# Optimization experiments

Measured on AMD Instinct MI355X. Metric: run time of the kernel, lower is better.

## Reference

```python
import jax, jax.numpy as jnp
import numpy as np

GZ = 15          # grid size (gz)
C_IN = 4         # grid channels == R output dim
N_DEEP = 16      # number of stride-1 conv blocks after conv1
BN_EPS = 1e-5


def _bn_eval(x, g, b):
    # eval-mode BatchNorm2d with running_mean=0, running_var=1
    s = g / jnp.sqrt(1.0 + BN_EPS)
    return x * s[None, :, None, None] + b[None, :, None, None]


def _conv(x, w, b, stride):
    y = jax.lax.conv_general_dilated(
        x, w, window_strides=(stride, stride), padding=[(2, 2), (2, 2)],
        dimension_numbers=('NCHW', 'OIHW', 'NCHW'))
    return y + b[None, :, None, None]


def _cnn(x, conv1_w, conv1_b, bn1_g, bn1_b, convs_w, convs_b, bns_g, bns_b):
    x = jax.nn.elu(_bn_eval(_conv(x, conv1_w, conv1_b, 2), bn1_g, bn1_b))
    for i in range(N_DEEP):  # fixed small layer count
        x = jax.nn.elu(_bn_eval(_conv(x, convs_w[i], convs_b[i], 1), bns_g[i], bns_b[i]))
    return x


def _per_example_mean(points, attrs, W1, b1, W2, b2, W3, b3,
                      conv1_w, conv1_b, bn1_g, bn1_b, convs_w, convs_b, bns_g, bns_b):
    # Disty: scalar euclidean distance from each point to its cell center, + attr -> 2 features
    cell = jnp.clip(jnp.floor(points), 0.0, GZ - 1.0).astype(jnp.int32)  # [N,2]
    center = cell.astype(points.dtype) + 0.5
    dist = jnp.sqrt(jnp.sum((points - center) ** 2, axis=-1, keepdims=True) + 1e-12)  # [N,1]
    h = jnp.concatenate([dist, attrs], axis=-1)  # [N,2]
    # R: per-point MLP 2->16->16->4
    h = jax.nn.elu(h @ W1 + b1)
    h = jax.nn.elu(h @ W2 + b2)
    feats = h @ W3 + b3  # [N,4]
    # Agg: scatter-max into the 15x15 grid by containing cell
    cid = cell[:, 0] * GZ + cell[:, 1]  # [N]
    grid = jnp.zeros((GZ * GZ, C_IN), points.dtype).at[cid].max(feats)
    x = grid.reshape(GZ, GZ, C_IN).transpose(2, 0, 1)[None]  # [1,4,15,15]
    out = _cnn(x, conv1_w, conv1_b, bn1_g, bn1_b, convs_w, convs_b, bns_g, bns_b)
    return out.mean()


def setup_inputs():
    key = jax.random.key(0)
    ks = jax.random.split(key, 20)
    B, N = 128, 16384
    inp = {
        'points': jax.random.uniform(ks[0], (B, N, 2), jnp.float32) * GZ,
        'attrs': jax.random.normal(ks[1], (B, N, 1), jnp.float32),
        'goal_force': jax.random.normal(ks[2], (B, N, 2), jnp.float32) * 0.01,
        'goal_attrs': jax.random.normal(ks[3], (B, N, 1), jnp.float32) * 0.01,
    }
    def lin(k, i, o):
        return jax.random.normal(k, (i, o), jnp.float32) / np.float32(np.sqrt(i))
    inp['W1'] = lin(ks[4], 2, 16);  inp['b1'] = jnp.zeros((16,), jnp.float32)
    inp['W2'] = lin(ks[5], 16, 16); inp['b2'] = jnp.zeros((16,), jnp.float32)
    inp['W3'] = lin(ks[6], 16, 4);  inp['b3'] = jnp.zeros((4,), jnp.float32)
    inp['conv1_w'] = jax.random.normal(ks[7], (32, 4, 5, 5), jnp.float32) / np.float32(np.sqrt(4 * 25))
    inp['conv1_b'] = jnp.zeros((32,), jnp.float32)
    inp['bn1_g'] = jnp.ones((32,), jnp.float32)
    inp['bn1_b'] = jnp.zeros((32,), jnp.float32)
    inp['convs_w'] = jax.random.normal(ks[8], (N_DEEP, 32, 32, 5, 5), jnp.float32) / np.float32(np.sqrt(32 * 25))
    inp['convs_b'] = jnp.zeros((N_DEEP, 32), jnp.float32)
    inp['bns_g'] = jnp.ones((N_DEEP, 32), jnp.float32)
    inp['bns_b'] = jnp.zeros((N_DEEP, 32), jnp.float32)
    return inp


def reference(points, attrs, goal_force, goal_attrs, W1, b1, W2, b2, W3, b3,
              conv1_w, conv1_b, bn1_g, bn1_b, convs_w, convs_b, bns_g, bns_b):
    f = lambda p, a: _per_example_mean(p, a, W1, b1, W2, b2, W3, b3,
                                       conv1_w, conv1_b, bn1_g, bn1_b,
                                       convs_w, convs_b, bns_g, bns_b)
    # per-example gradient of output[idx].mean() wrt points/attrs (the torch autograd.grad loop)
    dpoints, dattrs = jax.vmap(jax.grad(f, argnums=(0, 1)))(points, attrs)
    cost = ((dpoints - goal_force) ** 2).mean() + ((dattrs - goal_attrs) ** 2).mean()
    B = points.shape[0]
    g_sum = (dpoints.sum() + dattrs.sum()) / B
    g_abs_sum = (jnp.abs(dpoints).sum() + jnp.abs(dattrs).sum()) / B
    return cost, g_sum, g_abs_sum, dpoints, dattrs
```

## Files before the change

### kernel.cpp

```cpp
#include <hip/hip_runtime.h>

#define TPB 256


static __device__ __forceinline__ unsigned long long dkey(double d) {
  unsigned long long b = (unsigned long long)__double_as_longlong(d);
  return (b & 0x8000000000000000ull) ? ~b : (b | 0x8000000000000000ull);
}

static __device__ __forceinline__ double expm1_fast(double z) {
  double t = z * 1.4426950408889634;
  double k = rint(t);
  double r = fma(k, -6.9314718036912381649e-01, z);
  r = fma(k, -1.9082149292705877e-10, r);
  double p = 2.08767569878681e-09;
  p = fma(p, r, 2.505210838544172e-08);
  p = fma(p, r, 2.755731922398589e-07);
  p = fma(p, r, 2.7557319223985893e-06);
  p = fma(p, r, 2.48015873015873e-05);
  p = fma(p, r, 1.984126984126984e-04);
  p = fma(p, r, 1.388888888888889e-03);
  p = fma(p, r, 8.333333333333333e-03);
  p = fma(p, r, 4.1666666666666664e-02);
  p = fma(p, r, 1.6666666666666666e-01);
  p = fma(p, r, 5e-01);
  double q = fma(r * p, r, r);
  long long ki = (long long)k;
  double s = __longlong_as_double((unsigned long long)(1023LL + ki) << 52);
  return fma(s, q, s - 1.0);
}

static __device__ __forceinline__ void mlp_forward(
    float px, float py, float at,
    const float* __restrict__ W1, const float* __restrict__ b1,
    const float* __restrict__ W2, const float* __restrict__ b2,
    const float* __restrict__ W3, const float* __restrict__ b3,
    int& c0, int& c1, double& dx, double& dy, double& dist,
    double a1[16], double a2[16], double f[4]) {
  c0 = (int)floorf(px); c0 = c0 < 0 ? 0 : (c0 > 14 ? 14 : c0);
  c1 = (int)floorf(py); c1 = c1 < 0 ? 0 : (c1 > 14 ? 14 : c1);
  dx = (double)px - ((double)c0 + 0.5);
  dy = (double)py - ((double)c1 + 0.5);
  dist = sqrt(fma(dx, dx, fma(dy, dy, 1e-12)));
  double datt = (double)at;
#pragma unroll
  for (int j = 0; j < 16; ++j) {
    double z = fma(dist, (double)W1[j], fma(datt, (double)W1[16 + j], (double)b1[j]));
    a1[j] = z > 0.0 ? z : expm1_fast(z);
  }
#pragma unroll
  for (int j = 0; j < 16; ++j) {
    double z = (double)b2[j];
#pragma unroll
    for (int i = 0; i < 16; ++i) z = fma(a1[i], (double)W2[i * 16 + j], z);
    a2[j] = z > 0.0 ? z : expm1_fast(z);
  }
#pragma unroll
  for (int k = 0; k < 4; ++k) {
    double ff = (double)b3[k];
#pragma unroll
    for (int i = 0; i < 16; ++i) ff = fma(a2[i], (double)W3[i * 4 + k], ff);
    f[k] = ff;
  }
}

__global__ __launch_bounds__(TPB)
void k_init(unsigned long long* __restrict__ gp, unsigned int* __restrict__ widx) {
  int e = blockIdx.x * TPB + threadIdx.x;
  if (e < 128 * 900) { gp[e] = 0x8000000000000000ull; widx[e] = 0xFFFFFFFFu; }
}

__global__ __launch_bounds__(TPB)
void k_wtrans(const float* __restrict__ cw, float* __restrict__ wT, float* __restrict__ wTb) {
  int i = blockIdx.x * TPB + threadIdx.x;
  if (i >= 409600) return;
  int c = i & 7;
  int m = (i >> 3) & 31;
  int g = (i >> 8) & 3;
  int jt = i >> 10;
  int t = jt % 25;
  int j = jt / 25;
  wT[i]  = cw[((size_t)(j * 32 + (g * 8 + c)) * 32 + m) * 25 + t];
  wTb[i] = cw[((size_t)(j * 32 + m) * 32 + (g * 8 + c)) * 25 + (24 - t)];
}

__global__ __launch_bounds__(TPB)
void k_point_fwd(const float* __restrict__ points, const float* __restrict__ attrs,
                 const float* __restrict__ W1, const float* __restrict__ b1,
                 const float* __restrict__ W2, const float* __restrict__ b2,
                 const float* __restrict__ W3, const float* __restrict__ b3,
                 unsigned long long* __restrict__ gp) {
  int gid = blockIdx.x * TPB + threadIdx.x;
  float2 p2 = ((const float2*)points)[gid];
  float at = attrs[gid];
  int c0, c1; double dx, dy, dist, a1[16], a2[16], f[4];
  mlp_forward(p2.x, p2.y, at, W1, b1, W2, b2, W3, b3, c0, c1, dx, dy, dist, a1, a2, f);
  int b = gid >> 14;
  size_t base = (size_t)b * 900 + (size_t)(c0 * 15 + c1) * 4;
#pragma unroll
  for (int k = 0; k < 4; ++k) atomicMax(&gp[base + k], dkey(f[k]));
}

__global__ __launch_bounds__(TPB)
void k_claim(const float* __restrict__ points, const float* __restrict__ attrs,
             const float* __restrict__ W1, const float* __restrict__ b1,
             const float* __restrict__ W2, const float* __restrict__ b2,
             const float* __restrict__ W3, const float* __restrict__ b3,
             const unsigned long long* __restrict__ gp, unsigned int* __restrict__ widx) {
  int gid = blockIdx.x * TPB + threadIdx.x;
  float2 p2 = ((const float2*)points)[gid];
  float at = attrs[gid];
  int c0, c1; double dx, dy, dist, a1[16], a2[16], f[4];
  mlp_forward(p2.x, p2.y, at, W1, b1, W2, b2, W3, b3, c0, c1, dx, dy, dist, a1, a2, f);
  int b = gid >> 14;
  size_t base = (size_t)b * 900 + (size_t)(c0 * 15 + c1) * 4;
#pragma unroll
  for (int k = 0; k < 4; ++k)
    if (dkey(f[k]) == gp[base + k]) atomicMin(&widx[base + k], (unsigned)(gid & 16383));
}

static __device__ __forceinline__ void conv_mac8(const float* __restrict__ Rd, int rd_base,
                                                 const float* __restrict__ wb, float acc[8]) {
  int po = rd_base;
  const float* wp = wb;
#pragma unroll 1
  for (int ky = 0; ky < 5; ++ky) {
#pragma unroll 1
    for (int kx = 0; kx < 5; ++kx) {
      const float4 a0 = *(const float4*)&Rd[po];
      const float4 a1 = *(const float4*)&Rd[po + 4];
#pragma unroll
      for (int c = 0; c < 8; ++c) {
        acc[c] = fmaf(wp[c],      a0.x, acc[c]);
        acc[c] = fmaf(wp[8 + c],  a0.y, acc[c]);
        acc[c] = fmaf(wp[16 + c], a0.z, acc[c]);
        acc[c] = fmaf(wp[24 + c], a0.w, acc[c]);
        acc[c] = fmaf(wp[32 + c], a1.x, acc[c]);
        acc[c] = fmaf(wp[40 + c], a1.y, acc[c]);
        acc[c] = fmaf(wp[48 + c], a1.z, acc[c]);
        acc[c] = fmaf(wp[56 + c], a1.w, acc[c]);
      }
      po += 36; wp += 1024;
    }
    po += 7 * 36;
  }
}

__global__ __launch_bounds__(1024, 4)
void k_cnn_fwd(const unsigned long long* __restrict__ gp,
               const float* __restrict__ c1w, const float* __restrict__ c1b,
               const float* __restrict__ bn1g, const float* __restrict__ bn1b,
               const float* __restrict__ wT, const float* __restrict__ cb,
               const float* __restrict__ bg, const float* __restrict__ bb,
               float* __restrict__ acts) {
  __shared__ float xin[900];
  __shared__ __align__(16) float bufA[5184], bufB[5184];
  __shared__ __align__(16) float4 partA[768], partB[768];
  const int tid = threadIdx.x;
  const int b = blockIdx.x;
  for (int t = tid; t < 10368; t += 1024) {
    ((float*)bufA)[t < 5184 ? t : t] = 0.f;
  }
  for (int t = tid; t < 5184; t += 1024) { bufA[t] = 0.f; bufB[t] = 0.f; }
  if (tid < 900) {
    int c = tid / 225, rem = tid - c * 225;
    unsigned long long k = gp[(size_t)b * 900 + rem * 4 + c];
    long long bits = (k & 0x8000000000000000ull) ? (long long)(k & 0x7FFFFFFFFFFFFFFFull)
                                                 : ~(long long)k;
    xin[c * 225 + rem] = (float)__longlong_as_double(bits);
  }
  __syncthreads();
  const float irs = 1.0f / sqrtf(1.0f + 1e-5f);
  float* actE = acts + (size_t)b * 34816;
#pragma unroll
  for (int r = 0; r < 2; ++r) {
    int k = tid + r * 1024;
    int co = k >> 6, pix = k & 63, y = pix >> 3, x = pix & 7;
    float acc = c1b[co];
    for (int ci = 0; ci < 4; ++ci)
#pragma unroll
      for (int ky = 0; ky < 5; ++ky) {
        int iy = 2 * y + ky - 2;
        if (iy < 0 || iy > 14) continue;
#pragma unroll
        for (int kx = 0; kx < 5; ++kx) {
          int ix = 2 * x + kx - 2;
          if (ix < 0 || ix > 14) continue;
          acc = fmaf(c1w[((co * 4 + ci) * 5 + ky) * 5 + kx], xin[ci * 225 + iy * 15 + ix], acc);
        }
      }
    float z = fmaf(acc, bn1g[co] * irs, bn1b[co]);
    float a = z > 0.f ? z : expm1f(z);
    bufA[((y + 2) * 12 + (x + 2)) * 36 + co] = a;
    actE[pix * 32 + co] = a;
  }
  __syncthreads();
  const int w = __builtin_amdgcn_readfirstlane(tid >> 6);
  const int lane = tid & 63;
  const int g = w & 3, q = w >> 2;
  const int y = lane >> 3, x = lane & 7;
  const int rd_base = (y * 12 + x) * 36 + q * 8;
  const int st_pix = ((y + 2) * 12 + (x + 2)) * 36 + g * 8;
#pragma unroll 1
  for (int j = 0; j < 16; ++j) {
    const float* Rd = (j & 1) ? bufB : bufA;
    float* Wr = (j & 1) ? bufA : bufB;
    const float* wb = wT + (size_t)j * 25600 + g * 256 + q * 64;
    float acc[8] = {0.f, 0.f, 0.f, 0.f, 0.f, 0.f, 0.f, 0.f};
    conv_mac8(Rd, rd_base, wb, acc);
    if (q > 0) {
      int slot = ((q - 1) * 4 + g) * 64 + lane;
      partA[slot] = make_float4(acc[0], acc[1], acc[2], acc[3]);
      partB[slot] = make_float4(acc[4], acc[5], acc[6], acc[7]);
    }
    __syncthreads();
    if (q == 0) {
#pragma unroll
      for (int p = 0; p < 3; ++p) {
        float4 pa = partA[(p * 4 + g) * 64 + lane];
        float4 pb = partB[(p * 4 + g) * 64 + lane];
        acc[0] += pa.x; acc[1] += pa.y; acc[2] += pa.z; acc[3] += pa.w;
        acc[4] += pb.x; acc[5] += pb.y; acc[6] += pb.z; acc[7] += pb.w;
      }
      const int cbase = j * 32 + g * 8;
      float av[8];
#pragma unroll
      for (int c = 0; c < 8; ++c) {
        float z = fmaf(acc[c] + cb[cbase + c], bg[cbase + c] * irs, bb[cbase + c]);
        av[c] = z > 0.f ? z : expm1f(z);
      }
      *(float4*)&Wr[st_pix]     = make_float4(av[0], av[1], av[2], av[3]);
      *(float4*)&Wr[st_pix + 4] = make_float4(av[4], av[5], av[6], av[7]);
      float* ap = actE + (size_t)(j + 1) * 2048 + lane * 32 + g * 8;
      *(float4*)&ap[0] = make_float4(av[0], av[1], av[2], av[3]);
      *(float4*)&ap[4] = make_float4(av[4], av[5], av[6], av[7]);
    }
    __syncthreads();
  }
}

__global__ __launch_bounds__(1024, 4)
void k_cnn_bwd(const float* __restrict__ acts,
               const float* __restrict__ wTb, const float* __restrict__ bg,
               const float* __restrict__ c1w, const float* __restrict__ bn1g,
               float* __restrict__ dgrid) {
  __shared__ __align__(16) float bufA[5184], bufB[5184];
  __shared__ __align__(16) float4 partA[768], partB[768];
  const int tid = threadIdx.x;
  const int b = blockIdx.x;
  for (int t = tid; t < 5184; t += 1024) { bufA[t] = 0.f; bufB[t] = 0.f; }
  __syncthreads();
  const float irs = 1.0f / sqrtf(1.0f + 1e-5f);
  const float* actE = acts + (size_t)b * 34816;
#pragma unroll
  for (int r = 0; r < 2; ++r) {
    int t = tid + r * 1024;
    int ch = t & 31, pix = t >> 5;
    float a = actE[16 * 2048 + pix * 32 + ch];
    float d = (a > 0.f ? 1.f : a + 1.f) * (bg[15 * 32 + ch] * irs);
    bufA[((2 + (pix >> 3)) * 12 + 2 + (pix & 7)) * 36 + ch] = d * (1.0f / 2048.0f);
  }
  __syncthreads();
  const int w = __builtin_amdgcn_readfirstlane(tid >> 6);
  const int lane = tid & 63;
  const int g = w & 3, q = w >> 2;
  const int y = lane >> 3, x = lane & 7;
  const int rd_base = (y * 12 + x) * 36 + q * 8;
  const int st_pix = ((y + 2) * 12 + (x + 2)) * 36 + g * 8;
#pragma unroll 1
  for (int jj = 0; jj < 16; ++jj) {
    const int j = 15 - jj;
    const float* Gb = (jj & 1) ? bufB : bufA;
    float* Wr = (jj & 1) ? bufA : bufB;
    const float* wb = wTb + (size_t)j * 25600 + g * 256 + q * 64;
    float acc[8] = {0.f, 0.f, 0.f, 0.f, 0.f, 0.f, 0.f, 0.f};
    conv_mac8(Gb, rd_base, wb, acc);
    if (q > 0) {
      int slot = ((q - 1) * 4 + g) * 64 + lane;
      partA[slot] = make_float4(acc[0], acc[1], acc[2], acc[3]);
      partB[slot] = make_float4(acc[4], acc[5], acc[6], acc[7]);
    }
    __syncthreads();
    if (q == 0) {
#pragma unroll
      for (int p = 0; p < 3; ++p) {
        float4 pa = partA[(p * 4 + g) * 64 + lane];
        float4 pb = partB[(p * 4 + g) * 64 + lane];
        acc[0] += pa.x; acc[1] += pa.y; acc[2] += pa.z; acc[3] += pa.w;
        acc[4] += pb.x; acc[5] += pb.y; acc[6] += pb.z; acc[7] += pb.w;
      }
      const float* ap = actE + (size_t)j * 2048 + lane * 32 + g * 8;
      float4 A0 = *(const float4*)&ap[0];
      float4 A1 = *(const float4*)&ap[4];
      float avv[8] = {A0.x, A0.y, A0.z, A0.w, A1.x, A1.y, A1.z, A1.w};
#pragma unroll
      for (int c = 0; c < 8; ++c) {
        float s = (j > 0) ? bg[(j - 1) * 32 + g * 8 + c] : bn1g[g * 8 + c];
        acc[c] *= (avv[c] > 0.f ? 1.f : avv[c] + 1.f) * (s * irs);
      }
      *(float4*)&Wr[st_pix]     = make_float4(acc[0], acc[1], acc[2], acc[3]);
      *(float4*)&Wr[st_pix + 4] = make_float4(acc[4], acc[5], acc[6], acc[7]);
    }
    __syncthreads();
  }
  if (tid < 900) {
    int cid = tid >> 2, ci = tid & 3;
    int u = cid / 15, v = cid - u * 15;
    float acc = 0.f;
    for (int co = 0; co < 32; ++co) {
      const float* wp = c1w + (co * 4 + ci) * 25;
#pragma unroll
      for (int ky = 0; ky < 5; ++ky) {
        int t2 = u + 2 - ky;
        if (t2 < 0 || t2 > 14 || (t2 & 1)) continue;
        int yy = t2 >> 1;
#pragma unroll
        for (int kx = 0; kx < 5; ++kx) {
          int s2 = v + 2 - kx;
          if (s2 < 0 || s2 > 14 || (s2 & 1)) continue;
          int xq = s2 >> 1;
          acc = fmaf(wp[ky * 5 + kx], bufA[((yy + 2) * 12 + (xq + 2)) * 36 + co], acc);
        }
      }
    }
    dgrid[(size_t)b * 900 + tid] = acc;
  }
}

__global__ __launch_bounds__(TPB)
void k_winner(const float* __restrict__ points, const float* __restrict__ attrs,
              const float* __restrict__ W1, const float* __restrict__ b1,
              const float* __restrict__ W2, const float* __restrict__ b2,
              const float* __restrict__ W3, const float* __restrict__ b3,
              const unsigned int* __restrict__ widx, const float* __restrict__ dgrid,
              float* __restrict__ dpoints, float* __restrict__ dattrs) {
  int e = blockIdx.x * TPB + threadIdx.x;
  unsigned pi = widx[e];
  if (pi == 0xFFFFFFFFu) return;
  float g = dgrid[e];
  if (g == 0.f) return;
  int b = e / 900;
  int r = e - b * 900;
  int ch = r & 3;
  size_t pidx = ((size_t)b << 14) + pi;
  float px = points[2 * pidx], py = points[2 * pidx + 1], at = attrs[pidx];
  int c0, c1; double dx, dy, dist, a1[16], a2[16], f[4];
  mlp_forward(px, py, at, W1, b1, W2, b2, W3, b3, c0, c1, dx, dy, dist, a1, a2, f);
  double gz2[16];
#pragma unroll
  for (int i = 0; i < 16; ++i) {
    double ga2 = (double)g * (double)W3[i * 4 + ch];
    gz2[i] = ga2 * (a2[i] > 0.0 ? 1.0 : a2[i] + 1.0);
  }
  double gd = 0.0, gatt = 0.0;
#pragma unroll
  for (int i = 0; i < 16; ++i) {
    double ga1 = 0.0;
#pragma unroll
    for (int jj = 0; jj < 16; ++jj) ga1 = fma(gz2[jj], (double)W2[i * 16 + jj], ga1);
    double gz1 = ga1 * (a1[i] > 0.0 ? 1.0 : a1[i] + 1.0);
    gd = fma(gz1, (double)W1[i], gd);
    gatt = fma(gz1, (double)W1[16 + i], gatt);
  }
  double inv = 1.0 / dist;
  atomicAdd(&dpoints[2 * pidx], (float)(gd * dx * inv));
  atomicAdd(&dpoints[2 * pidx + 1], (float)(gd * dy * inv));
  atomicAdd(&dattrs[pidx], (float)gatt);
}

__global__ __launch_bounds__(TPB)
void k_reduce(const float* __restrict__ dpoints, const float* __restrict__ dattrs,
              const float* __restrict__ gforce, const float* __restrict__ gattr,
              float* __restrict__ out) {
  int i = blockIdx.x * TPB + threadIdx.x;
  float dp0 = dpoints[2 * i], dp1 = dpoints[2 * i + 1], da = dattrs[i];
  float gf0 = gforce[2 * i], gf1 = gforce[2 * i + 1], ga = gattr[i];
  float e0 = dp0 - gf0, e1 = dp1 - gf1, e2 = da - ga;
  float c1v = e0 * e0 + e1 * e1;
  float c2v = e2 * e2;
  float sm = dp0 + dp1 + da;
  float ab = fabsf(dp0) + fabsf(dp1) + fabsf(da);
#pragma unroll
  for (int o = 32; o > 0; o >>= 1) {
    c1v += __shfl_down(c1v, o, 64);
    c2v += __shfl_down(c2v, o, 64);
    sm += __shfl_down(sm, o, 64);
    ab += __shfl_down(ab, o, 64);
  }
  __shared__ float red[4][4];
  int wv = threadIdx.x >> 6, ln = threadIdx.x & 63;
  if (ln == 0) { red[wv][0] = c1v; red[wv][1] = c2v; red[wv][2] = sm; red[wv][3] = ab; }
  __syncthreads();
  if (threadIdx.x == 0) {
    float C1 = 0, C2 = 0, S = 0, A = 0;
    for (int w = 0; w < 4; ++w) { C1 += red[w][0]; C2 += red[w][1]; S += red[w][2]; A += red[w][3]; }
    atomicAdd(&out[0], C1 * (1.0f / 4194304.0f) + C2 * (1.0f / 2097152.0f));
    atomicAdd(&out[1], S * (1.0f / 128.0f));
    atomicAdd(&out[2], A * (1.0f / 128.0f));
  }
}

extern "C" void kernel_launch(void* const* d_in, const int* in_sizes, int n_in,
                              void* d_out, int out_size, void* d_ws, size_t ws_size,
                              hipStream_t stream) {
  (void)in_sizes; (void)n_in; (void)ws_size;
  const float* points = (const float*)d_in[0];
  const float* attrs  = (const float*)d_in[1];
  const float* gforce = (const float*)d_in[2];
  const float* gattr  = (const float*)d_in[3];
  const float* W1 = (const float*)d_in[4];
  const float* b1 = (const float*)d_in[5];
  const float* W2 = (const float*)d_in[6];
  const float* b2 = (const float*)d_in[7];
  const float* W3 = (const float*)d_in[8];
  const float* b3 = (const float*)d_in[9];
  const float* c1w  = (const float*)d_in[10];
  const float* c1b  = (const float*)d_in[11];
  const float* bn1g = (const float*)d_in[12];
  const float* bn1b = (const float*)d_in[13];
  const float* cw = (const float*)d_in[14];
  const float* cb = (const float*)d_in[15];
  const float* bg = (const float*)d_in[16];
  const float* bb = (const float*)d_in[17];
  float* out = (float*)d_out;

  char* ws = (char*)d_ws;
  unsigned long long* gp = (unsigned long long*)(ws);
  unsigned int* widx = (unsigned int*)(ws + 921600);
  float* dgrid = (float*)(ws + 1382400);
  float* wT  = (float*)(ws + 1843200);
  float* wTb = (float*)(ws + 3481600);
  float* acts = (float*)(ws + 5120000);

  float* dpoints = out + 3;
  float* dattrs  = out + 3 + 4194304;

  hipMemsetAsync(d_out, 0, (size_t)out_size * sizeof(float), stream);
  k_init<<<450, TPB, 0, stream>>>(gp, widx);
  k_wtrans<<<1600, TPB, 0, stream>>>(cw, wT, wTb);
  k_point_fwd<<<8192, TPB, 0, stream>>>(points, attrs, W1, b1, W2, b2, W3, b3, gp);
  k_claim<<<8192, TPB, 0, stream>>>(points, attrs, W1, b1, W2, b2, W3, b3, gp, widx);
  k_cnn_fwd<<<128, 1024, 0, stream>>>(gp, c1w, c1b, bn1g, bn1b, wT, cb, bg, bb, acts);
  k_cnn_bwd<<<128, 1024, 0, stream>>>(acts, wTb, bg, c1w, bn1g, dgrid);
  k_winner<<<450, TPB, 0, stream>>>(points, attrs, W1, b1, W2, b2, W3, b3, widx, dgrid,
                                    dpoints, dattrs);
  k_reduce<<<8192, TPB, 0, stream>>>(dpoints, dattrs, gforce, gattr, out);
}
```

Before: 1.327 ms.

## Filter scatter-max winners with fp32 pass, recompute only candidates in fp64

Replaces the two full fp64 MLP passes over all points with an fp32 max pass plus an fp32 candidate-selection pass that compacts points within a margin of the cell max into a list. Only those candidates are recomputed in fp64 to get the exact max and the winning index. This cuts the expensive double-precision work on most points, but adds a global atomic counter, an extra kernel, and relies on a fixed margin being wide enough to always contain the true fp64 winner. The candidate list shares workspace with the activation buffer, which is only written later.

```diff
diff --git a/kernel.cpp b/kernel.cpp
--- a/kernel.cpp
+++ b/kernel.cpp
@@ -1,11 +1,19 @@
 #include <hip/hip_runtime.h>
 
 #define TPB 256
+#define EPS_CAND 1e-3f
 
 
 static __device__ __forceinline__ unsigned long long dkey(double d) {
   unsigned long long b = (unsigned long long)__double_as_longlong(d);
   return (b & 0x8000000000000000ull) ? ~b : (b | 0x8000000000000000ull);
+}
+static __device__ __forceinline__ unsigned int key32(float f) {
+  unsigned int b = __float_as_uint(f);
+  return (b & 0x80000000u) ? ~b : (b | 0x80000000u);
+}
+static __device__ __forceinline__ float dec32(unsigned int k) {
+  return __uint_as_float((k & 0x80000000u) ? (k & 0x7FFFFFFFu) : ~k);
 }
 
 static __device__ __forceinline__ double expm1_fast(double z) {
@@ -64,10 +72,49 @@
   }
 }
 
-__global__ __launch_bounds__(TPB)
-void k_init(unsigned long long* __restrict__ gp, unsigned int* __restrict__ widx) {
+static __device__ __forceinline__ void mlp32(
+    float px, float py, float at,
+    const float* __restrict__ W1, const float* __restrict__ b1,
+    const float* __restrict__ W2, const float* __restrict__ b2,
+    const float* __restrict__ W3, const float* __restrict__ b3,
+    int& c0, int& c1, float f[4]) {
+  c0 = (int)floorf(px); c0 = c0 < 0 ? 0 : (c0 > 14 ? 14 : c0);
+  c1 = (int)floorf(py); c1 = c1 < 0 ? 0 : (c1 > 14 ? 14 : c1);
+  float dx = px - ((float)c0 + 0.5f);
+  float dy = py - ((float)c1 + 0.5f);
+  float dist = sqrtf(fmaf(dx, dx, fmaf(dy, dy, 1e-12f)));
+  float a1[16], a2[16];
+#pragma unroll
+  for (int j = 0; j < 16; ++j) {
+    float z = fmaf(dist, W1[j], fmaf(at, W1[16 + j], b1[j]));
+    a1[j] = z > 0.f ? z : expm1f(z);
+  }
+#pragma unroll
+  for (int j = 0; j < 16; ++j) {
+    float z = b2[j];
+#pragma unroll
+    for (int i = 0; i < 16; ++i) z = fmaf(a1[i], W2[i * 16 + j], z);
+    a2[j] = z > 0.f ? z : expm1f(z);
+  }
+#pragma unroll
+  for (int k = 0; k < 4; ++k) {
+    float ff = b3[k];
+#pragma unroll
+    for (int i = 0; i < 16; ++i) ff = fmaf(a2[i], W3[i * 4 + k], ff);
+    f[k] = ff;
+  }
+}
+
+__global__ __launch_bounds__(TPB)
+void k_init(unsigned long long* __restrict__ gp, unsigned int* __restrict__ widx,
+            unsigned int* __restrict__ gmax32, unsigned int* __restrict__ cnt) {
   int e = blockIdx.x * TPB + threadIdx.x;
-  if (e < 128 * 900) { gp[e] = 0x8000000000000000ull; widx[e] = 0xFFFFFFFFu; }
+  if (e < 128 * 900) {
+    gp[e] = 0x8000000000000000ull;
+    widx[e] = 0xFFFFFFFFu;
+    gmax32[e] = 0x80000000u;
+  }
+  if (e == 0) cnt[0] = 0;
 }
 
 __global__ __launch_bounds__(TPB)
@@ -85,38 +132,87 @@
 }
 
 __global__ __launch_bounds__(TPB)
-void k_point_fwd(const float* __restrict__ points, const float* __restrict__ attrs,
-                 const float* __restrict__ W1, const float* __restrict__ b1,
-                 const float* __restrict__ W2, const float* __restrict__ b2,
-                 const float* __restrict__ W3, const float* __restrict__ b3,
-                 unsigned long long* __restrict__ gp) {
+void k_pf32(const float* __restrict__ points, const float* __restrict__ attrs,
+            const float* __restrict__ W1, const float* __restrict__ b1,
+            const float* __restrict__ W2, const float* __restrict__ b2,
+            const float* __restrict__ W3, const float* __restrict__ b3,
+            unsigned int* __restrict__ gmax32) {
   int gid = blockIdx.x * TPB + threadIdx.x;
   float2 p2 = ((const float2*)points)[gid];
   float at = attrs[gid];
-  int c0, c1; double dx, dy, dist, a1[16], a2[16], f[4];
-  mlp_forward(p2.x, p2.y, at, W1, b1, W2, b2, W3, b3, c0, c1, dx, dy, dist, a1, a2, f);
+  int c0, c1; float f[4];
+  mlp32(p2.x, p2.y, at, W1, b1, W2, b2, W3, b3, c0, c1, f);
   int b = gid >> 14;
   size_t base = (size_t)b * 900 + (size_t)(c0 * 15 + c1) * 4;
 #pragma unroll
-  for (int k = 0; k < 4; ++k) atomicMax(&gp[base + k], dkey(f[k]));
-}
-
-__global__ __launch_bounds__(TPB)
-void k_claim(const float* __restrict__ points, const float* __restrict__ attrs,
-             const float* __restrict__ W1, const float* __restrict__ b1,
-             const float* __restrict__ W2, const float* __restrict__ b2,
-             const float* __restrict__ W3, const float* __restrict__ b3,
-             const unsigned long long* __restrict__ gp, unsigned int* __restrict__ widx) {
+  for (int k = 0; k < 4; ++k) atomicMax(&gmax32[base + k], key32(f[k]));
+}
+
+__global__ __launch_bounds__(TPB)
+void k_cand(const float* __restrict__ points, const float* __restrict__ attrs,
+            const float* __restrict__ W1, const float* __restrict__ b1,
+            const float* __restrict__ W2, const float* __restrict__ b2,
+            const float* __restrict__ W3, const float* __restrict__ b3,
+            const unsigned int* __restrict__ gmax32,
+            unsigned int* __restrict__ clist, unsigned int* __restrict__ cnt) {
   int gid = blockIdx.x * TPB + threadIdx.x;
   float2 p2 = ((const float2*)points)[gid];
   float at = attrs[gid];
-  int c0, c1; double dx, dy, dist, a1[16], a2[16], f[4];
-  mlp_forward(p2.x, p2.y, at, W1, b1, W2, b2, W3, b3, c0, c1, dx, dy, dist, a1, a2, f);
+  int c0, c1; float f[4];
+  mlp32(p2.x, p2.y, at, W1, b1, W2, b2, W3, b3, c0, c1, f);
   int b = gid >> 14;
   size_t base = (size_t)b * 900 + (size_t)(c0 * 15 + c1) * 4;
+  bool cand = false;
 #pragma unroll
   for (int k = 0; k < 4; ++k)
-    if (dkey(f[k]) == gp[base + k]) atomicMin(&widx[base + k], (unsigned)(gid & 16383));
+    cand |= (f[k] >= dec32(gmax32[base + k]) - EPS_CAND);
+  if (cand) {
+    unsigned pos = atomicAdd(cnt, 1u);
+    clist[pos] = (unsigned)gid;
+  }
+}
+
+__global__ __launch_bounds__(TPB)
+void k_pf64(const float* __restrict__ points, const float* __restrict__ attrs,
+            const float* __restrict__ W1, const float* __restrict__ b1,
+            const float* __restrict__ W2, const float* __restrict__ b2,
+            const float* __restrict__ W3, const float* __restrict__ b3,
+            const unsigned int* __restrict__ clist, const unsigned int* __restrict__ cnt,
+            unsigned long long* __restrict__ gp) {
+  int n = (int)cnt[0];
+  for (int i = blockIdx.x * TPB + threadIdx.x; i < n; i += gridDim.x * TPB) {
+    int gid = (int)clist[i];
+    float2 p2 = ((const float2*)points)[gid];
+    float at = attrs[gid];
+    int c0, c1; double dx, dy, dist, a1[16], a2[16], f[4];
+    mlp_forward(p2.x, p2.y, at, W1, b1, W2, b2, W3, b3, c0, c1, dx, dy, dist, a1, a2, f);
+    int b = gid >> 14;
+    size_t base = (size_t)b * 900 + (size_t)(c0 * 15 + c1) * 4;
+#pragma unroll
+    for (int k = 0; k < 4; ++k) atomicMax(&gp[base + k], dkey(f[k]));
+  }
+}
+
+__global__ __launch_bounds__(TPB)
+void k_claim64(const float* __restrict__ points, const float* __restrict__ attrs,
+               const float* __restrict__ W1, const float* __restrict__ b1,
+               const float* __restrict__ W2, const float* __restrict__ b2,
+               const float* __restrict__ W3, const float* __restrict__ b3,
+               const unsigned int* __restrict__ clist, const unsigned int* __restrict__ cnt,
+               const unsigned long long* __restrict__ gp, unsigned int* __restrict__ widx) {
+  int n = (int)cnt[0];
+  for (int i = blockIdx.x * TPB + threadIdx.x; i < n; i += gridDim.x * TPB) {
+    int gid = (int)clist[i];
+    float2 p2 = ((const float2*)points)[gid];
+    float at = attrs[gid];
+    int c0, c1; double dx, dy, dist, a1[16], a2[16], f[4];
+    mlp_forward(p2.x, p2.y, at, W1, b1, W2, b2, W3, b3, c0, c1, dx, dy, dist, a1, a2, f);
+    int b = gid >> 14;
+    size_t base = (size_t)b * 900 + (size_t)(c0 * 15 + c1) * 4;
+#pragma unroll
+    for (int k = 0; k < 4; ++k)
+      if (dkey(f[k]) == gp[base + k]) atomicMin(&widx[base + k], (unsigned)(gid & 16383));
+  }
 }
 
 static __device__ __forceinline__ void conv_mac8(const float* __restrict__ Rd, int rd_base,
@@ -158,9 +254,6 @@
   __shared__ __align__(16) float4 partA[768], partB[768];
   const int tid = threadIdx.x;
   const int b = blockIdx.x;
-  for (int t = tid; t < 10368; t += 1024) {
-    ((float*)bufA)[t < 5184 ? t : t] = 0.f;
-  }
   for (int t = tid; t < 5184; t += 1024) { bufA[t] = 0.f; bufB[t] = 0.f; }
   if (tid < 900) {
     int c = tid / 225, rem = tid - c * 225;
@@ -428,18 +521,23 @@
   unsigned long long* gp = (unsigned long long*)(ws);
   unsigned int* widx = (unsigned int*)(ws + 921600);
   float* dgrid = (float*)(ws + 1382400);
-  float* wT  = (float*)(ws + 1843200);
-  float* wTb = (float*)(ws + 3481600);
-  float* acts = (float*)(ws + 5120000);
+  unsigned int* gmax32 = (unsigned int*)(ws + 1843200);
+  unsigned int* cnt = (unsigned int*)(ws + 2304000);
+  float* wT  = (float*)(ws + 2305024);
+  float* wTb = (float*)(ws + 3943424);
+  unsigned int* clist = (unsigned int*)(ws + 5581824);
+  float* acts = (float*)(ws + 5581824);
 
   float* dpoints = out + 3;
   float* dattrs  = out + 3 + 4194304;
 
   hipMemsetAsync(d_out, 0, (size_t)out_size * sizeof(float), stream);
-  k_init<<<450, TPB, 0, stream>>>(gp, widx);
+  k_init<<<450, TPB, 0, stream>>>(gp, widx, gmax32, cnt);
   k_wtrans<<<1600, TPB, 0, stream>>>(cw, wT, wTb);
-  k_point_fwd<<<8192, TPB, 0, stream>>>(points, attrs, W1, b1, W2, b2, W3, b3, gp);
-  k_claim<<<8192, TPB, 0, stream>>>(points, attrs, W1, b1, W2, b2, W3, b3, gp, widx);
+  k_pf32<<<8192, TPB, 0, stream>>>(points, attrs, W1, b1, W2, b2, W3, b3, gmax32);
+  k_cand<<<8192, TPB, 0, stream>>>(points, attrs, W1, b1, W2, b2, W3, b3, gmax32, clist, cnt);
+  k_pf64<<<2048, TPB, 0, stream>>>(points, attrs, W1, b1, W2, b2, W3, b3, clist, cnt, gp);
+  k_claim64<<<2048, TPB, 0, stream>>>(points, attrs, W1, b1, W2, b2, W3, b3, clist, cnt, gp, widx);
   k_cnn_fwd<<<128, 1024, 0, stream>>>(gp, c1w, c1b, bn1g, bn1b, wT, cb, bg, bb, acts);
   k_cnn_bwd<<<128, 1024, 0, stream>>>(acts, wTb, bg, c1w, bn1g, dgrid);
   k_winner<<<450, TPB, 0, stream>>>(points, attrs, W1, b1, W2, b2, W3, b3, widx, dgrid,
```

New measurement: 1.855 ms. 39.8% more time.

## Pack winner index into scatter-max key and fuse CNN forward/backward kernels

Applied to the files above, without the earlier changes.

Packs the inverted point index into the low 14 bits of the double sort key, so one atomicMax pass gives both the max value and the lowest-index winner. This drops the second MLP recomputation pass (k_claim) and the widx buffer. The CNN forward and backward kernels are merged into one launch, keeping per-example state on chip. The risk is that truncating 14 mantissa bits of the double key can change tie-breaking or the max value slightly, and the fused kernel may use more registers.

```diff
diff --git a/kernel.cpp b/kernel.cpp
--- a/kernel.cpp
+++ b/kernel.cpp
@@ -65,9 +65,9 @@
 }
 
 __global__ __launch_bounds__(TPB)
-void k_init(unsigned long long* __restrict__ gp, unsigned int* __restrict__ widx) {
+void k_init(unsigned long long* __restrict__ gp) {
   int e = blockIdx.x * TPB + threadIdx.x;
-  if (e < 128 * 900) { gp[e] = 0x8000000000000000ull; widx[e] = 0xFFFFFFFFu; }
+  if (e < 128 * 900) gp[e] = 0x8000000000000000ull;
 }
 
 __global__ __launch_bounds__(TPB)
@@ -85,38 +85,22 @@
 }
 
 __global__ __launch_bounds__(TPB)
-void k_point_fwd(const float* __restrict__ points, const float* __restrict__ attrs,
-                 const float* __restrict__ W1, const float* __restrict__ b1,
-                 const float* __restrict__ W2, const float* __restrict__ b2,
-                 const float* __restrict__ W3, const float* __restrict__ b3,
-                 unsigned long long* __restrict__ gp) {
+void k_scatter(const float* __restrict__ points, const float* __restrict__ attrs,
+               const float* __restrict__ W1, const float* __restrict__ b1,
+               const float* __restrict__ W2, const float* __restrict__ b2,
+               const float* __restrict__ W3, const float* __restrict__ b3,
+               unsigned long long* __restrict__ gp) {
   int gid = blockIdx.x * TPB + threadIdx.x;
   float2 p2 = ((const float2*)points)[gid];
   float at = attrs[gid];
   int c0, c1; double dx, dy, dist, a1[16], a2[16], f[4];
   mlp_forward(p2.x, p2.y, at, W1, b1, W2, b2, W3, b3, c0, c1, dx, dy, dist, a1, a2, f);
   int b = gid >> 14;
+  unsigned long long inv = (unsigned long long)(16383 - (gid & 16383));
   size_t base = (size_t)b * 900 + (size_t)(c0 * 15 + c1) * 4;
 #pragma unroll
-  for (int k = 0; k < 4; ++k) atomicMax(&gp[base + k], dkey(f[k]));
-}
-
-__global__ __launch_bounds__(TPB)
-void k_claim(const float* __restrict__ points, const float* __restrict__ attrs,
-             const float* __restrict__ W1, const float* __restrict__ b1,
-             const float* __restrict__ W2, const float* __restrict__ b2,
-             const float* __restrict__ W3, const float* __restrict__ b3,
-             const unsigned long long* __restrict__ gp, unsigned int* __restrict__ widx) {
-  int gid = blockIdx.x * TPB + threadIdx.x;
-  float2 p2 = ((const float2*)points)[gid];
-  float at = attrs[gid];
-  int c0, c1; double dx, dy, dist, a1[16], a2[16], f[4];
-  mlp_forward(p2.x, p2.y, at, W1, b1, W2, b2, W3, b3, c0, c1, dx, dy, dist, a1, a2, f);
-  int b = gid >> 14;
-  size_t base = (size_t)b * 900 + (size_t)(c0 * 15 + c1) * 4;
-#pragma unroll
   for (int k = 0; k < 4; ++k)
-    if (dkey(f[k]) == gp[base + k]) atomicMin(&widx[base + k], (unsigned)(gid & 16383));
+    atomicMax(&gp[base + k], (dkey(f[k]) & 0xFFFFFFFFFFFFC000ull) | inv);
 }
 
 static __device__ __forceinline__ void conv_mac8(const float* __restrict__ Rd, int rd_base,
@@ -147,24 +131,22 @@
 }
 
 __global__ __launch_bounds__(1024, 4)
-void k_cnn_fwd(const unsigned long long* __restrict__ gp,
-               const float* __restrict__ c1w, const float* __restrict__ c1b,
-               const float* __restrict__ bn1g, const float* __restrict__ bn1b,
-               const float* __restrict__ wT, const float* __restrict__ cb,
-               const float* __restrict__ bg, const float* __restrict__ bb,
-               float* __restrict__ acts) {
+void k_cnn(const unsigned long long* __restrict__ gp,
+           const float* __restrict__ c1w, const float* __restrict__ c1b,
+           const float* __restrict__ bn1g, const float* __restrict__ bn1b,
+           const float* __restrict__ wT, const float* __restrict__ wTb,
+           const float* __restrict__ cb, const float* __restrict__ bg,
+           const float* __restrict__ bb,
+           float* __restrict__ acts, float* __restrict__ dgrid) {
   __shared__ float xin[900];
   __shared__ __align__(16) float bufA[5184], bufB[5184];
   __shared__ __align__(16) float4 partA[768], partB[768];
   const int tid = threadIdx.x;
   const int b = blockIdx.x;
-  for (int t = tid; t < 10368; t += 1024) {
-    ((float*)bufA)[t < 5184 ? t : t] = 0.f;
-  }
   for (int t = tid; t < 5184; t += 1024) { bufA[t] = 0.f; bufB[t] = 0.f; }
   if (tid < 900) {
     int c = tid / 225, rem = tid - c * 225;
-    unsigned long long k = gp[(size_t)b * 900 + rem * 4 + c];
+    unsigned long long k = gp[(size_t)b * 900 + rem * 4 + c] & 0xFFFFFFFFFFFFC000ull;
     long long bits = (k & 0x8000000000000000ull) ? (long long)(k & 0x7FFFFFFFFFFFFFFFull)
                                                  : ~(long long)k;
     xin[c * 225 + rem] = (float)__longlong_as_double(bits);
@@ -237,21 +219,6 @@
     }
     __syncthreads();
   }
-}
-
-__global__ __launch_bounds__(1024, 4)
-void k_cnn_bwd(const float* __restrict__ acts,
-               const float* __restrict__ wTb, const float* __restrict__ bg,
-               const float* __restrict__ c1w, const float* __restrict__ bn1g,
-               float* __restrict__ dgrid) {
-  __shared__ __align__(16) float bufA[5184], bufB[5184];
-  __shared__ __align__(16) float4 partA[768], partB[768];
-  const int tid = threadIdx.x;
-  const int b = blockIdx.x;
-  for (int t = tid; t < 5184; t += 1024) { bufA[t] = 0.f; bufB[t] = 0.f; }
-  __syncthreads();
-  const float irs = 1.0f / sqrtf(1.0f + 1e-5f);
-  const float* actE = acts + (size_t)b * 34816;
 #pragma unroll
   for (int r = 0; r < 2; ++r) {
     int t = tid + r * 1024;
@@ -261,12 +228,6 @@
     bufA[((2 + (pix >> 3)) * 12 + 2 + (pix & 7)) * 36 + ch] = d * (1.0f / 2048.0f);
   }
   __syncthreads();
-  const int w = __builtin_amdgcn_readfirstlane(tid >> 6);
-  const int lane = tid & 63;
-  const int g = w & 3, q = w >> 2;
-  const int y = lane >> 3, x = lane & 7;
-  const int rd_base = (y * 12 + x) * 36 + q * 8;
-  const int st_pix = ((y + 2) * 12 + (x + 2)) * 36 + g * 8;
 #pragma unroll 1
   for (int jj = 0; jj < 16; ++jj) {
     const int j = 15 - jj;
@@ -332,16 +293,17 @@
               const float* __restrict__ W1, const float* __restrict__ b1,
               const float* __restrict__ W2, const float* __restrict__ b2,
               const float* __restrict__ W3, const float* __restrict__ b3,
-              const unsigned int* __restrict__ widx, const float* __restrict__ dgrid,
+              const unsigned long long* __restrict__ gp, const float* __restrict__ dgrid,
               float* __restrict__ dpoints, float* __restrict__ dattrs) {
   int e = blockIdx.x * TPB + threadIdx.x;
-  unsigned pi = widx[e];
-  if (pi == 0xFFFFFFFFu) return;
+  unsigned long long pk = gp[e];
+  if (pk <= 0x8000000000000000ull) return;
   float g = dgrid[e];
   if (g == 0.f) return;
   int b = e / 900;
   int r = e - b * 900;
   int ch = r & 3;
+  int pi = 16383 - (int)(pk & 0x3FFFull);
   size_t pidx = ((size_t)b << 14) + pi;
   float px = points[2 * pidx], py = points[2 * pidx + 1], at = attrs[pidx];
   int c0, c1; double dx, dy, dist, a1[16], a2[16], f[4];
@@ -426,23 +388,20 @@
 
   char* ws = (char*)d_ws;
   unsigned long long* gp = (unsigned long long*)(ws);
-  unsigned int* widx = (unsigned int*)(ws + 921600);
-  float* dgrid = (float*)(ws + 1382400);
-  float* wT  = (float*)(ws + 1843200);
-  float* wTb = (float*)(ws + 3481600);
-  float* acts = (float*)(ws + 5120000);
+  float* dgrid = (float*)(ws + 921600);
+  float* wT  = (float*)(ws + 1382400);
+  float* wTb = (float*)(ws + 3020800);
+  float* acts = (float*)(ws + 4659200);
 
   float* dpoints = out + 3;
   float* dattrs  = out + 3 + 4194304;
 
   hipMemsetAsync(d_out, 0, (size_t)out_size * sizeof(float), stream);
-  k_init<<<450, TPB, 0, stream>>>(gp, widx);
+  k_init<<<450, TPB, 0, stream>>>(gp);
   k_wtrans<<<1600, TPB, 0, stream>>>(cw, wT, wTb);
-  k_point_fwd<<<8192, TPB, 0, stream>>>(points, attrs, W1, b1, W2, b2, W3, b3, gp);
-  k_claim<<<8192, TPB, 0, stream>>>(points, attrs, W1, b1, W2, b2, W3, b3, gp, widx);
-  k_cnn_fwd<<<128, 1024, 0, stream>>>(gp, c1w, c1b, bn1g, bn1b, wT, cb, bg, bb, acts);
-  k_cnn_bwd<<<128, 1024, 0, stream>>>(acts, wTb, bg, c1w, bn1g, dgrid);
-  k_winner<<<450, TPB, 0, stream>>>(points, attrs, W1, b1, W2, b2, W3, b3, widx, dgrid,
+  k_scatter<<<8192, TPB, 0, stream>>>(points, attrs, W1, b1, W2, b2, W3, b3, gp);
+  k_cnn<<<128, 1024, 0, stream>>>(gp, c1w, c1b, bn1g, bn1b, wT, wTb, cb, bg, bb, acts, dgrid);
+  k_winner<<<450, TPB, 0, stream>>>(points, attrs, W1, b1, W2, b2, W3, b3, gp, dgrid,
                                     dpoints, dattrs);
   k_reduce<<<8192, TPB, 0, stream>>>(dpoints, dattrs, gforce, gattr, out);
 }
```

Measured after the change: 1.212 ms. 8.7% less time.
